# Kernel optimization log

Hardware: AMD Instinct MI355X
Metric: run time of the kernel (lower is better)

The kernel has to match this reference:

```python
import jax, jax.numpy as jnp
import numpy as np

HEAD_NUM = 8
NEG_BIG = 1.0e9


def setup_inputs() -> dict:
    key = jax.random.key(0)
    ks = jax.random.split(key, 9)
    B, S, D = 8, 1024, 512
    return {
        "query": jax.random.normal(ks[0], (B, S, D), dtype=jnp.float32),
        "key": jax.random.normal(ks[1], (B, S, D), dtype=jnp.float32),
        "value": jax.random.normal(ks[2], (B, S, D), dtype=jnp.float32),
        "query_mask": jax.random.randint(ks[3], (B, S), 0, 2, dtype=jnp.int32),
        "key_mask": jax.random.randint(ks[4], (B, S), 0, 2, dtype=jnp.int32),
        "Wq": jax.random.normal(ks[5], (D, D), dtype=jnp.float32) * (1.0 / np.sqrt(D)),
        "Wk": jax.random.normal(ks[6], (D, D), dtype=jnp.float32) * (1.0 / np.sqrt(D)),
        "Wv": jax.random.normal(ks[7], (D, D), dtype=jnp.float32) * (1.0 / np.sqrt(D)),
        "Wo": jax.random.normal(ks[8], (D, D), dtype=jnp.float32) * (1.0 / np.sqrt(D)),
    }


def _split_heads(x, h):
    # TF: tf.concat(tf.split(x, h, axis=2), axis=0) -> (h*B, S, D//h), head-major rows
    return jnp.concatenate(jnp.split(x, h, axis=2), axis=0)


def reference(query, key, value, query_mask, key_mask, Wq, Wk, Wv, Wo):
    H = HEAD_NUM
    B, Sq, Dq = query.shape
    Sk = key.shape[1]
    D = value.shape[-1]

    q = query @ Wq   # (B, Sq, D)
    k = key @ Wk     # (B, Sk, D)
    v = value @ Wv   # (B, Sk, D)

    q_ = _split_heads(q, H)  # (H*B, Sq, D/H)
    k_ = _split_heads(k, H)
    v_ = _split_heads(v, H)

    # TF _reshape_mask: tile then reshape -> batch-major (b*H + h) rows (faithful)
    km = jnp.reshape(jnp.tile(key_mask[:, None, :], (1, H, 1)), (-1, Sk))

    sims = jnp.einsum('bqd,bkd->bqk', q_, k_) / jnp.sqrt(jnp.float32(Dq))

    # causal band mask (sequence_mask=True)
    ones = jnp.ones((Sq, Sk), dtype=jnp.float32)
    causal = ones - jnp.tril(ones)
    sims = sims - causal[None, :, :] * NEG_BIG

    # additive key padding mask
    sims = sims - (1.0 - km[:, None, :].astype(jnp.float32)) * NEG_BIG

    att = jax.nn.softmax(sims, axis=-1)            # (H*B, Sq, Sk)
    out = jnp.einsum('bqk,bkd->bqd', att, v_)      # (H*B, Sq, D/H)

    # faithful TF recombination: reshape (-1, H, Sq, D/H) -> transpose -> (-1, Sq, D)
    out = out.reshape(-1, H, Sq, D // H).transpose(0, 2, 1, 3).reshape(-1, Sq, D)

    out = out @ Wo
    out = jax.nn.relu(out)
    out = out * query_mask[:, :, None].astype(jnp.float32)
    return out
```

## Files before the change

### kernel.cpp

```cpp
#include <hip/hip_runtime.h>
#include <hip/hip_bf16.h>

typedef __bf16 bf16_t;
typedef __bf16 bf16x8 __attribute__((ext_vector_type(8)));
typedef float f32x4 __attribute__((ext_vector_type(4)));

#define CPOW 1.4426950409e9f
#define QSCALE 0.063758715f
#define MSTAT 16.0f

static __device__ __forceinline__ f32x4 mfma16x16x32(bf16x8 a, bf16x8 b, f32x4 c) {
    return __builtin_amdgcn_mfma_f32_16x16x32_bf16(a, b, c, 0, 0, 0);
}

__global__ __launch_bounds__(256, 2) void gemm_qkv(
        const float* __restrict__ Aq, const float* __restrict__ Ak, const float* __restrict__ Av,
        const float* __restrict__ Wq, const float* __restrict__ Wk, const float* __restrict__ Wv,
        bf16_t* __restrict__ Oq, bf16_t* __restrict__ Ok, bf16_t* __restrict__ Ov) {
    __shared__ bf16_t As[128][40];
    __shared__ bf16_t Bs[128][40];

    const int tid  = threadIdx.x;
    const int lane = tid & 63;
    const int wave = tid >> 6;
    const int l15  = lane & 15;
    const int kgrp = lane >> 4;
    const int wr   = wave >> 1;
    const int wc   = wave & 1;

    const int row0 = blockIdx.x * 128;
    const int col0 = blockIdx.y * 128;
    const int z    = blockIdx.z;

    const float* A = (z == 0) ? Aq : (z == 1) ? Ak : Av;
    const float* W = (z == 0) ? Wq : (z == 1) ? Wk : Wv;

    const int ar  = tid >> 1;
    const int ach = (tid & 1) * 16;
    const int bc  = tid & 127;
    const int bkh = (tid >> 7) * 16;

    f32x4 acc[4][4];
    #pragma unroll
    for (int m = 0; m < 4; ++m)
        #pragma unroll
        for (int n = 0; n < 4; ++n) acc[m][n] = (f32x4){0.f, 0.f, 0.f, 0.f};

    float4 areg[4];
    float  breg[16];
    const float* Abase = A + (size_t)(row0 + ar) * 512 + ach;
    const float* Wbase = W + (size_t)bkh * 512 + col0 + bc;

    #pragma unroll
    for (int i = 0; i < 4; ++i) areg[i] = *(const float4*)(Abase + i * 4);
    #pragma unroll
    for (int i = 0; i < 16; ++i) breg[i] = Wbase[(size_t)i * 512];

    for (int kb0 = 0; kb0 < 512; kb0 += 32) {
        __syncthreads();
        {
            bf16x8 w0, w1;
            #pragma unroll
            for (int i = 0; i < 4; ++i) { w0[i] = (bf16_t)(&areg[0].x)[i]; w0[i + 4] = (bf16_t)(&areg[1].x)[i]; }
            #pragma unroll
            for (int i = 0; i < 4; ++i) { w1[i] = (bf16_t)(&areg[2].x)[i]; w1[i + 4] = (bf16_t)(&areg[3].x)[i]; }
            *(bf16x8*)&As[ar][ach]     = w0;
            *(bf16x8*)&As[ar][ach + 8] = w1;
            bf16x8 b0, b1;
            #pragma unroll
            for (int i = 0; i < 8; ++i) { b0[i] = (bf16_t)breg[i]; b1[i] = (bf16_t)breg[i + 8]; }
            *(bf16x8*)&Bs[bc][bkh]     = b0;
            *(bf16x8*)&Bs[bc][bkh + 8] = b1;
        }
        __syncthreads();
        if (kb0 + 32 < 512) {
            const float* An = Abase + kb0 + 32;
            #pragma unroll
            for (int i = 0; i < 4; ++i) areg[i] = *(const float4*)(An + i * 4);
            const float* Wn = Wbase + (size_t)(kb0 + 32) * 512;
            #pragma unroll
            for (int i = 0; i < 16; ++i) breg[i] = Wn[(size_t)i * 512];
        }
        bf16x8 af[4], bf[4];
        #pragma unroll
        for (int m = 0; m < 4; ++m) af[m] = *(const bf16x8*)&As[wr * 64 + m * 16 + l15][kgrp * 8];
        #pragma unroll
        for (int n = 0; n < 4; ++n) bf[n] = *(const bf16x8*)&Bs[wc * 64 + n * 16 + l15][kgrp * 8];
        __builtin_amdgcn_s_setprio(1);
        #pragma unroll
        for (int m = 0; m < 4; ++m)
            #pragma unroll
            for (int n = 0; n < 4; ++n)
                acc[m][n] = mfma16x16x32(af[m], bf[n], acc[m][n]);
        __builtin_amdgcn_s_setprio(0);
    }

    bf16_t* O = (z == 0) ? Oq : (z == 1) ? Ok : Ov;
    const float esc = (z == 0) ? QSCALE : 1.0f;
    #pragma unroll
    for (int m = 0; m < 4; ++m)
        #pragma unroll
        for (int j = 0; j < 4; ++j) {
            const int r = row0 + wr * 64 + m * 16 + kgrp * 4 + j;
            #pragma unroll
            for (int n = 0; n < 4; ++n) {
                const int c = col0 + wc * 64 + n * 16 + l15;
                if (z < 2) {
                    O[(size_t)r * 512 + c] = (bf16_t)(acc[m][n][j] * esc);
                } else {
                    const int bb = r >> 10, ss = r & 1023;
                    O[((size_t)bb * 512 + c) * 1024 + ss] = (bf16_t)acc[m][n][j];
                }
            }
        }
}

__global__ __launch_bounds__(256, 2) void gemm_out(const bf16_t* __restrict__ Ab,
                                                   const float* __restrict__ W,
                                                   float* __restrict__ Out,
                                                   const int* __restrict__ qmask) {
    __shared__ bf16_t As[128][40];
    __shared__ bf16_t Bs[128][40];

    const int tid  = threadIdx.x;
    const int lane = tid & 63;
    const int wave = tid >> 6;
    const int l15  = lane & 15;
    const int kgrp = lane >> 4;
    const int wr   = wave >> 1;
    const int wc   = wave & 1;

    const int row0 = blockIdx.x * 128;
    const int col0 = blockIdx.y * 128;

    const int ar  = tid >> 1;
    const int ach = (tid & 1) * 16;
    const int bc  = tid & 127;
    const int bkh = (tid >> 7) * 16;

    f32x4 acc[4][4];
    #pragma unroll
    for (int m = 0; m < 4; ++m)
        #pragma unroll
        for (int n = 0; n < 4; ++n) acc[m][n] = (f32x4){0.f, 0.f, 0.f, 0.f};

    bf16x8 areg[2];
    float  breg[16];
    const bf16_t* Abase = Ab + (size_t)(row0 + ar) * 512 + ach;
    const float*  Wbase = W + (size_t)bkh * 512 + col0 + bc;

    areg[0] = *(const bf16x8*)Abase;
    areg[1] = *(const bf16x8*)(Abase + 8);
    #pragma unroll
    for (int i = 0; i < 16; ++i) breg[i] = Wbase[(size_t)i * 512];

    for (int kb0 = 0; kb0 < 512; kb0 += 32) {
        __syncthreads();
        *(bf16x8*)&As[ar][ach]     = areg[0];
        *(bf16x8*)&As[ar][ach + 8] = areg[1];
        {
            bf16x8 b0, b1;
            #pragma unroll
            for (int i = 0; i < 8; ++i) { b0[i] = (bf16_t)breg[i]; b1[i] = (bf16_t)breg[i + 8]; }
            *(bf16x8*)&Bs[bc][bkh]     = b0;
            *(bf16x8*)&Bs[bc][bkh + 8] = b1;
        }
        __syncthreads();
        if (kb0 + 32 < 512) {
            const bf16_t* An = Abase + kb0 + 32;
            areg[0] = *(const bf16x8*)An;
            areg[1] = *(const bf16x8*)(An + 8);
            const float* Wn = Wbase + (size_t)(kb0 + 32) * 512;
            #pragma unroll
            for (int i = 0; i < 16; ++i) breg[i] = Wn[(size_t)i * 512];
        }
        bf16x8 af[4], bf[4];
        #pragma unroll
        for (int m = 0; m < 4; ++m) af[m] = *(const bf16x8*)&As[wr * 64 + m * 16 + l15][kgrp * 8];
        #pragma unroll
        for (int n = 0; n < 4; ++n) bf[n] = *(const bf16x8*)&Bs[wc * 64 + n * 16 + l15][kgrp * 8];
        __builtin_amdgcn_s_setprio(1);
        #pragma unroll
        for (int m = 0; m < 4; ++m)
            #pragma unroll
            for (int n = 0; n < 4; ++n)
                acc[m][n] = mfma16x16x32(af[m], bf[n], acc[m][n]);
        __builtin_amdgcn_s_setprio(0);
    }

    #pragma unroll
    for (int m = 0; m < 4; ++m)
        #pragma unroll
        for (int j = 0; j < 4; ++j) {
            const int r = row0 + wr * 64 + m * 16 + kgrp * 4 + j;
            const float fq = (float)qmask[r];
            #pragma unroll
            for (int n = 0; n < 4; ++n) {
                const int c = col0 + wc * 64 + n * 16 + l15;
                Out[(size_t)r * 512 + c] = fmaxf(acc[m][n][j], 0.0f) * fq;
            }
        }
}

__global__ __launch_bounds__(256, 3) void attn_flash(const bf16_t* __restrict__ qb,
                                                     const bf16_t* __restrict__ kb,
                                                     const bf16_t* __restrict__ vtb,
                                                     const int* __restrict__ key_mask,
                                                     bf16_t* __restrict__ attout) {
    __shared__ char shbuf[19456];
    bf16_t (*P)[32][72]   = (bf16_t(*)[32][72])shbuf;
    bf16_t (*Omg)[32][72] = (bf16_t(*)[32][72])shbuf;
    float* mmg = (float*)(shbuf + 18432);
    float* lmg = (float*)(shbuf + 18432 + 512);

    const int tid  = threadIdx.x;
    const int lane = tid & 63;
    const int w    = tid >> 6;
    const int l15  = lane & 15;
    const int kgrp = lane >> 4;

    const int hb = blockIdx.x;
    const int h  = hb >> 3;
    const int b  = hb & 7;
    const int qw = (31 - (int)blockIdx.y) * 32;

    const size_t bS512 = (size_t)b * 1024 * 512;
    const int hoff = h * 64;
    const int* km = key_mask + h * 1024;

    int kmv = km[lane];
    unsigned long long bal = __ballot(kmv != 0);
    int first1 = bal ? (__ffsll(bal) - 1) : 64;
    const bool slow = (qw < first1);
    const int ntiles = slow ? 16 : ((qw + 95) >> 6);

    bf16x8 aq[2][2];
    #pragma unroll
    for (int rf = 0; rf < 2; ++rf)
        #pragma unroll
        for (int ks = 0; ks < 2; ++ks)
            aq[rf][ks] = *(const bf16x8*)(qb + bS512 + (size_t)(qw + rf * 16 + l15) * 512
                                          + hoff + ks * 32 + kgrp * 8);

    f32x4 O[2][4];
    float m[2][4], l[2][4];
    #pragma unroll
    for (int rf = 0; rf < 2; ++rf) {
        #pragma unroll
        for (int df = 0; df < 4; ++df) O[rf][df] = (f32x4){0.f, 0.f, 0.f, 0.f};
        #pragma unroll
        for (int j = 0; j < 4; ++j) { m[rf][j] = slow ? -3.0e38f : MSTAT; l[rf][j] = 0.f; }
    }

    const bf16_t* kbase = kb + bS512 + hoff;
    const bf16_t* vbase = vtb + ((size_t)b * 512 + hoff) * 1024;

    for (int kt = w; kt < ntiles; kt += 4) {
        const int kt0 = kt * 64;

        f32x4 S[2][4];
        #pragma unroll
        for (int rf = 0; rf < 2; ++rf)
            #pragma unroll
            for (int cf = 0; cf < 4; ++cf) S[rf][cf] = (f32x4){0.f, 0.f, 0.f, 0.f};

        __builtin_amdgcn_s_setprio(1);
        #pragma unroll
        for (int cf = 0; cf < 4; ++cf) {
            const bf16_t* krow = kbase + (size_t)(kt0 + cf * 16 + l15) * 512 + kgrp * 8;
            bf16x8 bk0 = *(const bf16x8*)krow;
            bf16x8 bk1 = *(const bf16x8*)(krow + 32);
            S[0][cf] = mfma16x16x32(aq[0][0], bk0, S[0][cf]);
            S[0][cf] = mfma16x16x32(aq[0][1], bk1, S[0][cf]);
            S[1][cf] = mfma16x16x32(aq[1][0], bk0, S[1][cf]);
            S[1][cf] = mfma16x16x32(aq[1][1], bk1, S[1][cf]);
        }
        __builtin_amdgcn_s_setprio(0);

        float kmadd[4];
        #pragma unroll
        for (int cf = 0; cf < 4; ++cf)
            kmadd[cf] = (km[kt0 + cf * 16 + l15] == 0) ? CPOW : 0.0f;

        const bool needC = (kt0 + 63 > qw);

        if (!slow) {
            #pragma unroll
            for (int rf = 0; rf < 2; ++rf)
                #pragma unroll
                for (int j = 0; j < 4; ++j) {
                    const int qrow = qw + rf * 16 + kgrp * 4 + j;
                    float ps = 0.f;
                    #pragma unroll
                    for (int cf = 0; cf < 4; ++cf) {
                        float sub = kmadd[cf] + MSTAT;
                        if (needC && (kt0 + cf * 16 + l15 > qrow)) sub += CPOW;
                        float p = __builtin_amdgcn_exp2f(S[rf][cf][j] - sub);
                        S[rf][cf][j] = p;
                        ps += p;
                    }
                    l[rf][j] += ps;
                }
        } else {
            float mx[2][4];
            #pragma unroll
            for (int rf = 0; rf < 2; ++rf)
                #pragma unroll
                for (int j = 0; j < 4; ++j) {
                    const int qrow = qw + rf * 16 + kgrp * 4 + j;
                    float mj = -3.0e38f;
                    #pragma unroll
                    for (int cf = 0; cf < 4; ++cf) {
                        float sub = kmadd[cf];
                        if (kt0 + cf * 16 + l15 > qrow) sub += CPOW;
                        float s = S[rf][cf][j] - sub;
                        S[rf][cf][j] = s;
                        mj = fmaxf(mj, s);
                    }
                    mx[rf][j] = mj;
                }
            #pragma unroll
            for (int off = 1; off < 16; off <<= 1)
                #pragma unroll
                for (int rf = 0; rf < 2; ++rf)
                    #pragma unroll
                    for (int j = 0; j < 4; ++j)
                        mx[rf][j] = fmaxf(mx[rf][j], __shfl_xor(mx[rf][j], off));

            float fac[2][4];
            #pragma unroll
            for (int rf = 0; rf < 2; ++rf)
                #pragma unroll
                for (int j = 0; j < 4; ++j) {
                    float mn = fmaxf(m[rf][j], mx[rf][j]);
                    fac[rf][j] = __builtin_amdgcn_exp2f(m[rf][j] - mn);
                    m[rf][j] = mn;
                }
            #pragma unroll
            for (int rf = 0; rf < 2; ++rf)
                #pragma unroll
                for (int j = 0; j < 4; ++j) {
                    float ps = 0.f;
                    #pragma unroll
                    for (int cf = 0; cf < 4; ++cf) {
                        float p = __builtin_amdgcn_exp2f(S[rf][cf][j] - m[rf][j]);
                        S[rf][cf][j] = p;
                        ps += p;
                    }
                    l[rf][j] = l[rf][j] * fac[rf][j] + ps;
                }
            #pragma unroll
            for (int rf = 0; rf < 2; ++rf)
                #pragma unroll
                for (int df = 0; df < 4; ++df)
                    #pragma unroll
                    for (int j = 0; j < 4; ++j)
                        O[rf][df][j] *= fac[rf][j];
        }

        #pragma unroll
        for (int rf = 0; rf < 2; ++rf)
            #pragma unroll
            for (int cf = 0; cf < 4; ++cf)
                #pragma unroll
                for (int j = 0; j < 4; ++j)
                    P[w][rf * 16 + kgrp * 4 + j][cf * 16 + l15] = (bf16_t)S[rf][cf][j];
        asm volatile("s_waitcnt lgkmcnt(0)" ::: "memory");

        bf16x8 pa[2][2];
        #pragma unroll
        for (int rf = 0; rf < 2; ++rf)
            #pragma unroll
            for (int ks = 0; ks < 2; ++ks)
                pa[rf][ks] = *(const bf16x8*)&P[w][rf * 16 + l15][ks * 32 + kgrp * 8];

        __builtin_amdgcn_s_setprio(1);
        #pragma unroll
        for (int df = 0; df < 4; ++df) {
            const bf16_t* vrow = vbase + (size_t)(df * 16 + l15) * 1024 + kt0 + kgrp * 8;
            bf16x8 vf0 = *(const bf16x8*)vrow;
            bf16x8 vf1 = *(const bf16x8*)(vrow + 32);
            O[0][df] = mfma16x16x32(pa[0][0], vf0, O[0][df]);
            O[0][df] = mfma16x16x32(pa[0][1], vf1, O[0][df]);
            O[1][df] = mfma16x16x32(pa[1][0], vf0, O[1][df]);
            O[1][df] = mfma16x16x32(pa[1][1], vf1, O[1][df]);
        }
        __builtin_amdgcn_s_setprio(0);
    }

    __syncthreads();

    #pragma unroll
    for (int rf = 0; rf < 2; ++rf)
        #pragma unroll
        for (int j = 0; j < 4; ++j) {
            float lv = l[rf][j];
            #pragma unroll
            for (int off = 1; off < 16; off <<= 1) lv += __shfl_xor(lv, off);
            l[rf][j] = lv;
        }

    #pragma unroll
    for (int rf = 0; rf < 2; ++rf)
        #pragma unroll
        for (int df = 0; df < 4; ++df)
            #pragma unroll
            for (int j = 0; j < 4; ++j)
                Omg[w][rf * 16 + kgrp * 4 + j][df * 16 + l15] = (bf16_t)O[rf][df][j];
    if (l15 == 0) {
        #pragma unroll
        for (int rf = 0; rf < 2; ++rf)
            #pragma unroll
            for (int j = 0; j < 4; ++j) {
                mmg[w * 32 + rf * 16 + kgrp * 4 + j] = m[rf][j];
                lmg[w * 32 + rf * 16 + kgrp * 4 + j] = l[rf][j];
            }
    }
    __syncthreads();

    {
        const int r  = tid >> 3;
        const int c0 = (tid & 7) * 8;
        float m0 = mmg[r], m1 = mmg[32 + r], m2 = mmg[64 + r], m3 = mmg[96 + r];
        float M = fmaxf(fmaxf(m0, m1), fmaxf(m2, m3));
        float f0 = __builtin_amdgcn_exp2f(m0 - M), f1 = __builtin_amdgcn_exp2f(m1 - M);
        float f2 = __builtin_amdgcn_exp2f(m2 - M), f3 = __builtin_amdgcn_exp2f(m3 - M);
        float ls = lmg[r] * f0 + lmg[32 + r] * f1 + lmg[64 + r] * f2 + lmg[96 + r] * f3;
        float inv = 1.0f / ls;
        bf16x8 o0 = *(const bf16x8*)&Omg[0][r][c0];
        bf16x8 o1 = *(const bf16x8*)&Omg[1][r][c0];
        bf16x8 o2 = *(const bf16x8*)&Omg[2][r][c0];
        bf16x8 o3 = *(const bf16x8*)&Omg[3][r][c0];
        bf16_t outv[8];
        #pragma unroll
        for (int i = 0; i < 8; ++i) {
            float acc = (float)o0[i] * f0 + (float)o1[i] * f1
                      + (float)o2[i] * f2 + (float)o3[i] * f3;
            outv[i] = (bf16_t)(acc * inv);
        }
        *(bf16x8*)&attout[(size_t)(h * 1024 + qw + r) * 512 + b * 64 + c0] = *(bf16x8*)outv;
    }
}

extern "C" void kernel_launch(void* const* d_in, const int* in_sizes, int n_in,
                              void* d_out, int out_size, void* d_ws, size_t ws_size,
                              hipStream_t stream) {
    const float* query = (const float*)d_in[0];
    const float* key   = (const float*)d_in[1];
    const float* value = (const float*)d_in[2];
    const int*   qmask = (const int*)d_in[3];
    const int*   kmask = (const int*)d_in[4];
    const float* Wq    = (const float*)d_in[5];
    const float* Wk    = (const float*)d_in[6];
    const float* Wv    = (const float*)d_in[7];
    const float* Wo    = (const float*)d_in[8];
    float* out = (float*)d_out;

    const size_t NELEM = (size_t)8 * 1024 * 512;
    bf16_t* qb  = (bf16_t*)d_ws;
    bf16_t* kb  = qb + NELEM;
    bf16_t* vtb = kb + NELEM;
    bf16_t* ab  = vtb + NELEM;

    gemm_qkv<<<dim3(64, 4, 3), dim3(256), 0, stream>>>(query, key, value, Wq, Wk, Wv, qb, kb, vtb);
    attn_flash<<<dim3(64, 32), dim3(256), 0, stream>>>(qb, kb, vtb, kmask, ab);
    gemm_out<<<dim3(64, 4), dim3(256), 0, stream>>>(ab, Wo, out, qmask);
}
```

Before: 114.9 us.

## Shrink attention query tile from 32 to 16 rows and double the grid

Each attention block now handles 16 query rows instead of 32, and the grid doubles to 64x64 blocks. Register and shared-memory use per block roughly halve, and the causal tile count tracks the query position more finely. This aims at more parallelism, better occupancy and less wasted work on masked tiles. In exchange, every K/V tile is loaded twice as often across blocks and each loaded K/V fragment feeds half as many MFMAs, so arithmetic intensity drops.

```diff
diff --git a/kernel.cpp b/kernel.cpp
--- a/kernel.cpp
+++ b/kernel.cpp
@@ -2,6 +2,7 @@
 #include <hip/hip_bf16.h>
 
 typedef __bf16 bf16_t;
+typedef __bf16 bf16x4 __attribute__((ext_vector_type(4)));
 typedef __bf16 bf16x8 __attribute__((ext_vector_type(8)));
 typedef float f32x4 __attribute__((ext_vector_type(4)));
 
@@ -202,16 +203,16 @@
         }
 }
 
-__global__ __launch_bounds__(256, 3) void attn_flash(const bf16_t* __restrict__ qb,
-                                                     const bf16_t* __restrict__ kb,
-                                                     const bf16_t* __restrict__ vtb,
-                                                     const int* __restrict__ key_mask,
-                                                     bf16_t* __restrict__ attout) {
-    __shared__ char shbuf[19456];
-    bf16_t (*P)[32][72]   = (bf16_t(*)[32][72])shbuf;
-    bf16_t (*Omg)[32][72] = (bf16_t(*)[32][72])shbuf;
-    float* mmg = (float*)(shbuf + 18432);
-    float* lmg = (float*)(shbuf + 18432 + 512);
+__global__ __launch_bounds__(256) void attn_flash(const bf16_t* __restrict__ qb,
+                                                  const bf16_t* __restrict__ kb,
+                                                  const bf16_t* __restrict__ vtb,
+                                                  const int* __restrict__ key_mask,
+                                                  bf16_t* __restrict__ attout) {
+    __shared__ char shbuf[9728];
+    bf16_t (*P)[16][72]   = (bf16_t(*)[16][72])shbuf;
+    bf16_t (*Omg)[16][72] = (bf16_t(*)[16][72])shbuf;
+    float* mmg = (float*)(shbuf + 9216);
+    float* lmg = (float*)(shbuf + 9216 + 256);
 
     const int tid  = threadIdx.x;
     const int lane = tid & 63;
@@ -222,7 +223,7 @@
     const int hb = blockIdx.x;
     const int h  = hb >> 3;
     const int b  = hb & 7;
-    const int qw = (31 - (int)blockIdx.y) * 32;
+    const int q0 = (63 - (int)blockIdx.y) * 16;
 
     const size_t bS512 = (size_t)b * 1024 * 512;
     const int hoff = h * 64;
@@ -231,26 +232,21 @@
     int kmv = km[lane];
     unsigned long long bal = __ballot(kmv != 0);
     int first1 = bal ? (__ffsll(bal) - 1) : 64;
-    const bool slow = (qw < first1);
-    const int ntiles = slow ? 16 : ((qw + 95) >> 6);
-
-    bf16x8 aq[2][2];
-    #pragma unroll
-    for (int rf = 0; rf < 2; ++rf)
-        #pragma unroll
-        for (int ks = 0; ks < 2; ++ks)
-            aq[rf][ks] = *(const bf16x8*)(qb + bS512 + (size_t)(qw + rf * 16 + l15) * 512
-                                          + hoff + ks * 32 + kgrp * 8);
-
-    f32x4 O[2][4];
-    float m[2][4], l[2][4];
-    #pragma unroll
-    for (int rf = 0; rf < 2; ++rf) {
-        #pragma unroll
-        for (int df = 0; df < 4; ++df) O[rf][df] = (f32x4){0.f, 0.f, 0.f, 0.f};
-        #pragma unroll
-        for (int j = 0; j < 4; ++j) { m[rf][j] = slow ? -3.0e38f : MSTAT; l[rf][j] = 0.f; }
-    }
+    const bool slow = (q0 < first1);
+    const int ntiles = slow ? 16 : ((q0 + 79) >> 6);
+
+    bf16x8 aq[2];
+    #pragma unroll
+    for (int ks = 0; ks < 2; ++ks)
+        aq[ks] = *(const bf16x8*)(qb + bS512 + (size_t)(q0 + l15) * 512
+                                  + hoff + ks * 32 + kgrp * 8);
+
+    f32x4 O[4];
+    float m[4], l[4];
+    #pragma unroll
+    for (int df = 0; df < 4; ++df) O[df] = (f32x4){0.f, 0.f, 0.f, 0.f};
+    #pragma unroll
+    for (int j = 0; j < 4; ++j) { m[j] = slow ? -3.0e38f : MSTAT; l[j] = 0.f; }
 
     const bf16_t* kbase = kb + bS512 + hoff;
     const bf16_t* vbase = vtb + ((size_t)b * 512 + hoff) * 1024;
@@ -258,11 +254,9 @@
     for (int kt = w; kt < ntiles; kt += 4) {
         const int kt0 = kt * 64;
 
-        f32x4 S[2][4];
-        #pragma unroll
-        for (int rf = 0; rf < 2; ++rf)
-            #pragma unroll
-            for (int cf = 0; cf < 4; ++cf) S[rf][cf] = (f32x4){0.f, 0.f, 0.f, 0.f};
+        f32x4 S[4];
+        #pragma unroll
+        for (int cf = 0; cf < 4; ++cf) S[cf] = (f32x4){0.f, 0.f, 0.f, 0.f};
 
         __builtin_amdgcn_s_setprio(1);
         #pragma unroll
@@ -270,10 +264,8 @@
             const bf16_t* krow = kbase + (size_t)(kt0 + cf * 16 + l15) * 512 + kgrp * 8;
             bf16x8 bk0 = *(const bf16x8*)krow;
             bf16x8 bk1 = *(const bf16x8*)(krow + 32);
-            S[0][cf] = mfma16x16x32(aq[0][0], bk0, S[0][cf]);
-            S[0][cf] = mfma16x16x32(aq[0][1], bk1, S[0][cf]);
-            S[1][cf] = mfma16x16x32(aq[1][0], bk0, S[1][cf]);
-            S[1][cf] = mfma16x16x32(aq[1][1], bk1, S[1][cf]);
+            S[cf] = mfma16x16x32(aq[0], bk0, S[cf]);
+            S[cf] = mfma16x16x32(aq[1], bk1, S[cf]);
         }
         __builtin_amdgcn_s_setprio(0);
 
@@ -282,97 +274,81 @@
         for (int cf = 0; cf < 4; ++cf)
             kmadd[cf] = (km[kt0 + cf * 16 + l15] == 0) ? CPOW : 0.0f;
 
-        const bool needC = (kt0 + 63 > qw);
+        const bool needC = (kt0 + 63 > q0);
 
         if (!slow) {
             #pragma unroll
-            for (int rf = 0; rf < 2; ++rf)
+            for (int j = 0; j < 4; ++j) {
+                const int qrow = q0 + kgrp * 4 + j;
+                float ps = 0.f;
                 #pragma unroll
-                for (int j = 0; j < 4; ++j) {
-                    const int qrow = qw + rf * 16 + kgrp * 4 + j;
-                    float ps = 0.f;
-                    #pragma unroll
-                    for (int cf = 0; cf < 4; ++cf) {
-                        float sub = kmadd[cf] + MSTAT;
-                        if (needC && (kt0 + cf * 16 + l15 > qrow)) sub += CPOW;
-                        float p = __builtin_amdgcn_exp2f(S[rf][cf][j] - sub);
-                        S[rf][cf][j] = p;
-                        ps += p;
-                    }
-                    l[rf][j] += ps;
+                for (int cf = 0; cf < 4; ++cf) {
+                    float sub = kmadd[cf] + MSTAT;
+                    if (needC && (kt0 + cf * 16 + l15 > qrow)) sub += CPOW;
+                    float p = __builtin_amdgcn_exp2f(S[cf][j] - sub);
+                    S[cf][j] = p;
+                    ps += p;
                 }
+                l[j] += ps;
+            }
         } else {
-            float mx[2][4];
-            #pragma unroll
-            for (int rf = 0; rf < 2; ++rf)
+            float mx[4];
+            #pragma unroll
+            for (int j = 0; j < 4; ++j) {
+                const int qrow = q0 + kgrp * 4 + j;
+                float mj = -3.0e38f;
                 #pragma unroll
-                for (int j = 0; j < 4; ++j) {
-                    const int qrow = qw + rf * 16 + kgrp * 4 + j;
-                    float mj = -3.0e38f;
-                    #pragma unroll
-                    for (int cf = 0; cf < 4; ++cf) {
-                        float sub = kmadd[cf];
-                        if (kt0 + cf * 16 + l15 > qrow) sub += CPOW;
-                        float s = S[rf][cf][j] - sub;
-                        S[rf][cf][j] = s;
-                        mj = fmaxf(mj, s);
-                    }
-                    mx[rf][j] = mj;
+                for (int cf = 0; cf < 4; ++cf) {
+                    float sub = kmadd[cf];
+                    if (kt0 + cf * 16 + l15 > qrow) sub += CPOW;
+                    float s = S[cf][j] - sub;
+                    S[cf][j] = s;
+                    mj = fmaxf(mj, s);
                 }
+                mx[j] = mj;
+            }
             #pragma unroll
             for (int off = 1; off < 16; off <<= 1)
                 #pragma unroll
-                for (int rf = 0; rf < 2; ++rf)
-                    #pragma unroll
-                    for (int j = 0; j < 4; ++j)
-                        mx[rf][j] = fmaxf(mx[rf][j], __shfl_xor(mx[rf][j], off));
-
-            float fac[2][4];
-            #pragma unroll
-            for (int rf = 0; rf < 2; ++rf)
+                for (int j = 0; j < 4; ++j)
+                    mx[j] = fmaxf(mx[j], __shfl_xor(mx[j], off));
+
+            float fac[4];
+            #pragma unroll
+            for (int j = 0; j < 4; ++j) {
+                float mn = fmaxf(m[j], mx[j]);
+                fac[j] = __builtin_amdgcn_exp2f(m[j] - mn);
+                m[j] = mn;
+            }
+            #pragma unroll
+            for (int j = 0; j < 4; ++j) {
+                float ps = 0.f;
                 #pragma unroll
-                for (int j = 0; j < 4; ++j) {
-                    float mn = fmaxf(m[rf][j], mx[rf][j]);
-                    fac[rf][j] = __builtin_amdgcn_exp2f(m[rf][j] - mn);
-                    m[rf][j] = mn;
+                for (int cf = 0; cf < 4; ++cf) {
+                    float p = __builtin_amdgcn_exp2f(S[cf][j] - m[j]);
+                    S[cf][j] = p;
+                    ps += p;
                 }
-            #pragma unroll
-            for (int rf = 0; rf < 2; ++rf)
-                #pragma unroll
-                for (int j = 0; j < 4; ++j) {
-                    float ps = 0.f;
-                    #pragma unroll
-                    for (int cf = 0; cf < 4; ++cf) {
-                        float p = __builtin_amdgcn_exp2f(S[rf][cf][j] - m[rf][j]);
-                        S[rf][cf][j] = p;
-                        ps += p;
-                    }
-                    l[rf][j] = l[rf][j] * fac[rf][j] + ps;
-                }
-            #pragma unroll
-            for (int rf = 0; rf < 2; ++rf)
-                #pragma unroll
-                for (int df = 0; df < 4; ++df)
-                    #pragma unroll
-                    for (int j = 0; j < 4; ++j)
-                        O[rf][df][j] *= fac[rf][j];
-        }
-
-        #pragma unroll
-        for (int rf = 0; rf < 2; ++rf)
-            #pragma unroll
-            for (int cf = 0; cf < 4; ++cf)
+                l[j] = l[j] * fac[j] + ps;
+            }
+            #pragma unroll
+            for (int df = 0; df < 4; ++df)
                 #pragma unroll
                 for (int j = 0; j < 4; ++j)
-                    P[w][rf * 16 + kgrp * 4 + j][cf * 16 + l15] = (bf16_t)S[rf][cf][j];
+                    O[df][j] *= fac[j];
+        }
+
+        #pragma unroll
+        for (int cf = 0; cf < 4; ++cf)
+            #pragma unroll
+            for (int j = 0; j < 4; ++j)
+                P[w][kgrp * 4 + j][cf * 16 + l15] = (bf16_t)S[cf][j];
         asm volatile("s_waitcnt lgkmcnt(0)" ::: "memory");
 
-        bf16x8 pa[2][2];
-        #pragma unroll
-        for (int rf = 0; rf < 2; ++rf)
-            #pragma unroll
-            for (int ks = 0; ks < 2; ++ks)
-                pa[rf][ks] = *(const bf16x8*)&P[w][rf * 16 + l15][ks * 32 + kgrp * 8];
+        bf16x8 pa[2];
+        #pragma unroll
+        for (int ks = 0; ks < 2; ++ks)
+            pa[ks] = *(const bf16x8*)&P[w][l15][ks * 32 + kgrp * 8];
 
         __builtin_amdgcn_s_setprio(1);
         #pragma unroll
@@ -380,10 +356,8 @@
             const bf16_t* vrow = vbase + (size_t)(df * 16 + l15) * 1024 + kt0 + kgrp * 8;
             bf16x8 vf0 = *(const bf16x8*)vrow;
             bf16x8 vf1 = *(const bf16x8*)(vrow + 32);
-            O[0][df] = mfma16x16x32(pa[0][0], vf0, O[0][df]);
-            O[0][df] = mfma16x16x32(pa[0][1], vf1, O[0][df]);
-            O[1][df] = mfma16x16x32(pa[1][0], vf0, O[1][df]);
-            O[1][df] = mfma16x16x32(pa[1][1], vf1, O[1][df]);
+            O[df] = mfma16x16x32(pa[0], vf0, O[df]);
+            O[df] = mfma16x16x32(pa[1], vf1, O[df]);
         }
         __builtin_amdgcn_s_setprio(0);
     }
@@ -391,54 +365,48 @@
     __syncthreads();
 
     #pragma unroll
-    for (int rf = 0; rf < 2; ++rf)
+    for (int j = 0; j < 4; ++j) {
+        float lv = l[j];
+        #pragma unroll
+        for (int off = 1; off < 16; off <<= 1) lv += __shfl_xor(lv, off);
+        l[j] = lv;
+    }
+
+    #pragma unroll
+    for (int df = 0; df < 4; ++df)
+        #pragma unroll
+        for (int j = 0; j < 4; ++j)
+            Omg[w][kgrp * 4 + j][df * 16 + l15] = (bf16_t)O[df][j];
+    if (l15 == 0) {
         #pragma unroll
         for (int j = 0; j < 4; ++j) {
-            float lv = l[rf][j];
-            #pragma unroll
-            for (int off = 1; off < 16; off <<= 1) lv += __shfl_xor(lv, off);
-            l[rf][j] = lv;
-        }
-
-    #pragma unroll
-    for (int rf = 0; rf < 2; ++rf)
-        #pragma unroll
-        for (int df = 0; df < 4; ++df)
-            #pragma unroll
-            for (int j = 0; j < 4; ++j)
-                Omg[w][rf * 16 + kgrp * 4 + j][df * 16 + l15] = (bf16_t)O[rf][df][j];
-    if (l15 == 0) {
-        #pragma unroll
-        for (int rf = 0; rf < 2; ++rf)
-            #pragma unroll
-            for (int j = 0; j < 4; ++j) {
-                mmg[w * 32 + rf * 16 + kgrp * 4 + j] = m[rf][j];
-                lmg[w * 32 + rf * 16 + kgrp * 4 + j] = l[rf][j];
-            }
+            mmg[w * 16 + kgrp * 4 + j] = m[j];
+            lmg[w * 16 + kgrp * 4 + j] = l[j];
+        }
     }
     __syncthreads();
 
     {
-        const int r  = tid >> 3;
-        const int c0 = (tid & 7) * 8;
-        float m0 = mmg[r], m1 = mmg[32 + r], m2 = mmg[64 + r], m3 = mmg[96 + r];
+        const int r  = tid >> 4;
+        const int c0 = (tid & 15) * 4;
+        float m0 = mmg[r], m1 = mmg[16 + r], m2 = mmg[32 + r], m3 = mmg[48 + r];
         float M = fmaxf(fmaxf(m0, m1), fmaxf(m2, m3));
         float f0 = __builtin_amdgcn_exp2f(m0 - M), f1 = __builtin_amdgcn_exp2f(m1 - M);
         float f2 = __builtin_amdgcn_exp2f(m2 - M), f3 = __builtin_amdgcn_exp2f(m3 - M);
-        float ls = lmg[r] * f0 + lmg[32 + r] * f1 + lmg[64 + r] * f2 + lmg[96 + r] * f3;
+        float ls = lmg[r] * f0 + lmg[16 + r] * f1 + lmg[32 + r] * f2 + lmg[48 + r] * f3;
         float inv = 1.0f / ls;
-        bf16x8 o0 = *(const bf16x8*)&Omg[0][r][c0];
-        bf16x8 o1 = *(const bf16x8*)&Omg[1][r][c0];
-        bf16x8 o2 = *(const bf16x8*)&Omg[2][r][c0];
-        bf16x8 o3 = *(const bf16x8*)&Omg[3][r][c0];
-        bf16_t outv[8];
-        #pragma unroll
-        for (int i = 0; i < 8; ++i) {
+        bf16x4 o0 = *(const bf16x4*)&Omg[0][r][c0];
+        bf16x4 o1 = *(const bf16x4*)&Omg[1][r][c0];
+        bf16x4 o2 = *(const bf16x4*)&Omg[2][r][c0];
+        bf16x4 o3 = *(const bf16x4*)&Omg[3][r][c0];
+        bf16_t outv[4];
+        #pragma unroll
+        for (int i = 0; i < 4; ++i) {
             float acc = (float)o0[i] * f0 + (float)o1[i] * f1
                       + (float)o2[i] * f2 + (float)o3[i] * f3;
             outv[i] = (bf16_t)(acc * inv);
         }
-        *(bf16x8*)&attout[(size_t)(h * 1024 + qw + r) * 512 + b * 64 + c0] = *(bf16x8*)outv;
+        *(bf16x4*)&attout[(size_t)(h * 1024 + q0 + r) * 512 + b * 64 + c0] = *(bf16x4*)outv;
     }
 }
 
@@ -463,6 +431,6 @@
     bf16_t* ab  = vtb + NELEM;
 
     gemm_qkv<<<dim3(64, 4, 3), dim3(256), 0, stream>>>(query, key, value, Wq, Wk, Wv, qb, kb, vtb);
-    attn_flash<<<dim3(64, 32), dim3(256), 0, stream>>>(qb, kb, vtb, kmask, ab);
+    attn_flash<<<dim3(64, 64), dim3(256), 0, stream>>>(qb, kb, vtb, kmask, ab);
     gemm_out<<<dim3(64, 4), dim3(256), 0, stream>>>(ab, Wo, out, qmask);
 }
```

Measured after the change: 136.0 us. +18.3%, slower.

## Double-buffer K fragments in registers and issue V loads before softmax

Applied to the files above, without the earlier changes.

Each wave preloads its first K tile into registers, then, while processing each tile, prefetches the next tile's K fragments into a second register buffer. The loop is unrolled by two with swapped buffers. V fragments are now loaded right after the QK^T MFMAs, before the softmax, so global-load latency is hidden behind the exp/softmax work. This raises register pressure (extra K and V fragment arrays) under launch_bounds(256,2), which could cause spills or lower occupancy.

```diff
diff --git a/kernel.cpp b/kernel.cpp
--- a/kernel.cpp
+++ b/kernel.cpp
@@ -255,32 +255,54 @@
     const bf16_t* kbase = kb + bS512 + hoff;
     const bf16_t* vbase = vtb + ((size_t)b * 512 + hoff) * 1024;
 
-    for (int kt = w; kt < ntiles; kt += 4) {
+    bf16x8 kA[4][2], kB[4][2];
+    #pragma unroll
+    for (int cf = 0; cf < 4; ++cf) {
+        const bf16_t* krow = kbase + (size_t)(w * 64 + cf * 16 + l15) * 512 + kgrp * 8;
+        kA[cf][0] = *(const bf16x8*)krow;
+        kA[cf][1] = *(const bf16x8*)(krow + 32);
+    }
+
+    auto tile = [&](int kt, bf16x8 (&kc)[4][2], bf16x8 (&kn)[4][2]) {
         const int kt0 = kt * 64;
-
-        f32x4 S[2][4];
-        #pragma unroll
-        for (int rf = 0; rf < 2; ++rf)
-            #pragma unroll
-            for (int cf = 0; cf < 4; ++cf) S[rf][cf] = (f32x4){0.f, 0.f, 0.f, 0.f};
-
-        __builtin_amdgcn_s_setprio(1);
-        #pragma unroll
-        for (int cf = 0; cf < 4; ++cf) {
-            const bf16_t* krow = kbase + (size_t)(kt0 + cf * 16 + l15) * 512 + kgrp * 8;
-            bf16x8 bk0 = *(const bf16x8*)krow;
-            bf16x8 bk1 = *(const bf16x8*)(krow + 32);
-            S[0][cf] = mfma16x16x32(aq[0][0], bk0, S[0][cf]);
-            S[0][cf] = mfma16x16x32(aq[0][1], bk1, S[0][cf]);
-            S[1][cf] = mfma16x16x32(aq[1][0], bk0, S[1][cf]);
-            S[1][cf] = mfma16x16x32(aq[1][1], bk1, S[1][cf]);
-        }
-        __builtin_amdgcn_s_setprio(0);
 
         float kmadd[4];
         #pragma unroll
         for (int cf = 0; cf < 4; ++cf)
             kmadd[cf] = (km[kt0 + cf * 16 + l15] == 0) ? CPOW : 0.0f;
+
+        f32x4 S[2][4];
+        #pragma unroll
+        for (int rf = 0; rf < 2; ++rf)
+            #pragma unroll
+            for (int cf = 0; cf < 4; ++cf) S[rf][cf] = (f32x4){0.f, 0.f, 0.f, 0.f};
+
+        __builtin_amdgcn_s_setprio(1);
+        #pragma unroll
+        for (int cf = 0; cf < 4; ++cf) {
+            S[0][cf] = mfma16x16x32(aq[0][0], kc[cf][0], S[0][cf]);
+            S[0][cf] = mfma16x16x32(aq[0][1], kc[cf][1], S[0][cf]);
+            S[1][cf] = mfma16x16x32(aq[1][0], kc[cf][0], S[1][cf]);
+            S[1][cf] = mfma16x16x32(aq[1][1], kc[cf][1], S[1][cf]);
+        }
+        __builtin_amdgcn_s_setprio(0);
+
+        if (kt + 4 < ntiles) {
+            const int nt0 = kt0 + 256;
+            #pragma unroll
+            for (int cf = 0; cf < 4; ++cf) {
+                const bf16_t* krow = kbase + (size_t)(nt0 + cf * 16 + l15) * 512 + kgrp * 8;
+                kn[cf][0] = *(const bf16x8*)krow;
+                kn[cf][1] = *(const bf16x8*)(krow + 32);
+            }
+        }
+        bf16x8 vf[4][2];
+        #pragma unroll
+        for (int df = 0; df < 4; ++df) {
+            const bf16_t* vrow = vbase + (size_t)(df * 16 + l15) * 1024 + kt0 + kgrp * 8;
+            vf[df][0] = *(const bf16x8*)vrow;
+            vf[df][1] = *(const bf16x8*)(vrow + 32);
+        }
 
         const bool needC = (kt0 + 63 > qw);
 
@@ -377,15 +399,17 @@
         __builtin_amdgcn_s_setprio(1);
         #pragma unroll
         for (int df = 0; df < 4; ++df) {
-            const bf16_t* vrow = vbase + (size_t)(df * 16 + l15) * 1024 + kt0 + kgrp * 8;
-            bf16x8 vf0 = *(const bf16x8*)vrow;
-            bf16x8 vf1 = *(const bf16x8*)(vrow + 32);
-            O[0][df] = mfma16x16x32(pa[0][0], vf0, O[0][df]);
-            O[0][df] = mfma16x16x32(pa[0][1], vf1, O[0][df]);
-            O[1][df] = mfma16x16x32(pa[1][0], vf0, O[1][df]);
-            O[1][df] = mfma16x16x32(pa[1][1], vf1, O[1][df]);
+            O[0][df] = mfma16x16x32(pa[0][0], vf[df][0], O[0][df]);
+            O[0][df] = mfma16x16x32(pa[0][1], vf[df][1], O[0][df]);
+            O[1][df] = mfma16x16x32(pa[1][0], vf[df][0], O[1][df]);
+            O[1][df] = mfma16x16x32(pa[1][1], vf[df][1], O[1][df]);
         }
         __builtin_amdgcn_s_setprio(0);
+    };
+
+    for (int kt = w; kt < ntiles; kt += 8) {
+        tile(kt, kA, kB);
+        if (kt + 4 < ntiles) tile(kt + 4, kB, kA);
     }
 
     __syncthreads();
```

Result: slower. 219.1 us (+90.6%).

## Split attention key tiles across eight waves per block instead of four

Applied to the files above, without the earlier changes.

The flash attention kernel now launches 512 threads per block, so eight waves stride over key tiles instead of four, and shared memory for partial outputs and stats is doubled. The final merge combines eight partial softmax states per row, with each thread handling four columns. The aim is to shorten the per-block serial loop over key tiles for the causal workload. In exchange it adds merge work and shared memory, and with launch_bounds(512) it may lower block occupancy and raise register pressure.

```diff
diff --git a/kernel.cpp b/kernel.cpp
--- a/kernel.cpp
+++ b/kernel.cpp
@@ -2,6 +2,7 @@
 #include <hip/hip_bf16.h>
 
 typedef __bf16 bf16_t;
+typedef __bf16 bf16x4 __attribute__((ext_vector_type(4)));
 typedef __bf16 bf16x8 __attribute__((ext_vector_type(8)));
 typedef float f32x4 __attribute__((ext_vector_type(4)));
 
@@ -202,16 +203,16 @@
         }
 }
 
-__global__ __launch_bounds__(256, 3) void attn_flash(const bf16_t* __restrict__ qb,
-                                                     const bf16_t* __restrict__ kb,
-                                                     const bf16_t* __restrict__ vtb,
-                                                     const int* __restrict__ key_mask,
-                                                     bf16_t* __restrict__ attout) {
-    __shared__ char shbuf[19456];
+__global__ __launch_bounds__(512) void attn_flash(const bf16_t* __restrict__ qb,
+                                                  const bf16_t* __restrict__ kb,
+                                                  const bf16_t* __restrict__ vtb,
+                                                  const int* __restrict__ key_mask,
+                                                  bf16_t* __restrict__ attout) {
+    __shared__ char shbuf[38912];
     bf16_t (*P)[32][72]   = (bf16_t(*)[32][72])shbuf;
     bf16_t (*Omg)[32][72] = (bf16_t(*)[32][72])shbuf;
-    float* mmg = (float*)(shbuf + 18432);
-    float* lmg = (float*)(shbuf + 18432 + 512);
+    float* mmg = (float*)(shbuf + 36864);
+    float* lmg = (float*)(shbuf + 36864 + 1024);
 
     const int tid  = threadIdx.x;
     const int lane = tid & 63;
@@ -255,7 +256,7 @@
     const bf16_t* kbase = kb + bS512 + hoff;
     const bf16_t* vbase = vtb + ((size_t)b * 512 + hoff) * 1024;
 
-    for (int kt = w; kt < ntiles; kt += 4) {
+    for (int kt = w; kt < ntiles; kt += 8) {
         const int kt0 = kt * 64;
 
         f32x4 S[2][4];
@@ -419,26 +420,30 @@
     __syncthreads();
 
     {
-        const int r  = tid >> 3;
-        const int c0 = (tid & 7) * 8;
-        float m0 = mmg[r], m1 = mmg[32 + r], m2 = mmg[64 + r], m3 = mmg[96 + r];
-        float M = fmaxf(fmaxf(m0, m1), fmaxf(m2, m3));
-        float f0 = __builtin_amdgcn_exp2f(m0 - M), f1 = __builtin_amdgcn_exp2f(m1 - M);
-        float f2 = __builtin_amdgcn_exp2f(m2 - M), f3 = __builtin_amdgcn_exp2f(m3 - M);
-        float ls = lmg[r] * f0 + lmg[32 + r] * f1 + lmg[64 + r] * f2 + lmg[96 + r] * f3;
-        float inv = 1.0f / ls;
-        bf16x8 o0 = *(const bf16x8*)&Omg[0][r][c0];
-        bf16x8 o1 = *(const bf16x8*)&Omg[1][r][c0];
-        bf16x8 o2 = *(const bf16x8*)&Omg[2][r][c0];
-        bf16x8 o3 = *(const bf16x8*)&Omg[3][r][c0];
-        bf16_t outv[8];
-        #pragma unroll
-        for (int i = 0; i < 8; ++i) {
-            float acc = (float)o0[i] * f0 + (float)o1[i] * f1
-                      + (float)o2[i] * f2 + (float)o3[i] * f3;
-            outv[i] = (bf16_t)(acc * inv);
-        }
-        *(bf16x8*)&attout[(size_t)(h * 1024 + qw + r) * 512 + b * 64 + c0] = *(bf16x8*)outv;
+        const int r  = tid >> 4;
+        const int c0 = (tid & 15) * 4;
+        float M = -3.0e38f;
+        #pragma unroll
+        for (int s = 0; s < 8; ++s) M = fmaxf(M, mmg[s * 32 + r]);
+        float facs[8];
+        float ls = 0.f;
+        #pragma unroll
+        for (int s = 0; s < 8; ++s) {
+            facs[s] = __builtin_amdgcn_exp2f(mmg[s * 32 + r] - M);
+            ls += lmg[s * 32 + r] * facs[s];
+        }
+        const float inv = 1.0f / ls;
+        float acc[4] = {0.f, 0.f, 0.f, 0.f};
+        #pragma unroll
+        for (int s = 0; s < 8; ++s) {
+            bf16x4 o = *(const bf16x4*)&Omg[s][r][c0];
+            #pragma unroll
+            for (int i = 0; i < 4; ++i) acc[i] += (float)o[i] * facs[s];
+        }
+        bf16_t outv[4];
+        #pragma unroll
+        for (int i = 0; i < 4; ++i) outv[i] = (bf16_t)(acc[i] * inv);
+        *(bf16x4*)&attout[(size_t)(h * 1024 + qw + r) * 512 + b * 64 + c0] = *(bf16x4*)outv;
     }
 }
 
@@ -463,6 +468,6 @@
     bf16_t* ab  = vtb + NELEM;
 
     gemm_qkv<<<dim3(64, 4, 3), dim3(256), 0, stream>>>(query, key, value, Wq, Wk, Wv, qb, kb, vtb);
-    attn_flash<<<dim3(64, 32), dim3(256), 0, stream>>>(qb, kb, vtb, kmask, ab);
+    attn_flash<<<dim3(64, 32), dim3(512), 0, stream>>>(qb, kb, vtb, kmask, ab);
     gemm_out<<<dim3(64, 4), dim3(256), 0, stream>>>(ab, Wo, out, qmask);
 }
```

New measurement: 127.3 us. 10.7% more time.
